# Kernel optimization log

Measured on AMD Instinct MI355X. Metric: run time of the kernel, lower is better.

## Reference

```python
import jax, jax.numpy as jnp
import numpy as np
from jax import lax

B, CIN, COUT, H, W, K = 32, 256, 256, 56, 56, 3

def setup_inputs() -> dict:
    key = jax.random.key(0)
    k1, k2, k3 = jax.random.split(key, 3)
    inp = jax.random.normal(k1, (B, CIN, H, W), dtype=jnp.float32)
    # kaiming-style init for conv kernel, normal init for bias
    fan_in = CIN * K * K
    kernel = jax.random.normal(k2, (COUT, CIN, K, K), dtype=jnp.float32) * np.float32(np.sqrt(2.0 / fan_in))
    bias = jax.random.normal(k3, (COUT,), dtype=jnp.float32)
    return {"inp": inp, "kernel": kernel, "bias": bias}

def reference(inp, kernel, bias):
    # Equivalent to the crossbar path: im2col 3x3 patches @ stacked [kernel|bias]
    # matrix == standard conv2d(padding=1, stride=1) + bias.
    out = lax.conv_general_dilated(
        inp, kernel,
        window_strides=(1, 1),
        padding=((1, 1), (1, 1)),
        dimension_numbers=("NCHW", "OIHW", "NCHW"),
    )
    return out + bias[None, :, None, None]
```

## Files before the change

### kernel.cpp

```cpp
#include <hip/hip_runtime.h>
#include <hip/hip_bf16.h>


#define BB   32
#define CINC 256
#define COUTC 256
#define HH   56
#define WW   56
#define HP   58
#define WP   58
#define PIX_PER_IMG (HH*WW)
#define NPIX (BB*PIX_PER_IMG)
#define KTOT (9*CINC)
#define KB_STEPS (KTOT/32)

#define XT_ELEMS ((size_t)BB*HP*WP*CINC)
#define XT_BYTES (XT_ELEMS*2)
#define WR_ELEMS ((size_t)COUTC*KTOT)
#define WR_BYTES (WR_ELEMS*2)

#define BM 128
#define BN 128
#define BK 32

using frag_t = __attribute__((ext_vector_type(8))) short;
using f32x4  = __attribute__((ext_vector_type(4))) float;

__device__ __forceinline__ void gload_lds16(const void* gsrc, void* ldst) {
  __builtin_amdgcn_global_load_lds(
      (const __attribute__((address_space(1))) unsigned*)gsrc,
      (__attribute__((address_space(3))) unsigned*)ldst, 16, 0, 0);
}

__global__ void xpose_kernel(const float* __restrict__ inp,
                             __hip_bfloat16* __restrict__ xt) {
  int bid = blockIdx.x;
  int hp = bid % HP;
  int t  = bid / HP;
  int cb = t % 4;
  int b  = t / 4;
  __shared__ __hip_bfloat16 tile[64 * 60];
  int tid = threadIdx.x;
  for (int i = tid; i < 64 * 60; i += 256) tile[i] = __float2bfloat16(0.f);
  __syncthreads();
  int h = hp - 1;
  if (h >= 0 && h < HH) {
    const float* src = inp + ((size_t)(b * CINC + cb * 64) * HH + h) * WW;
    for (int i = tid; i < 64 * WW; i += 256) {
      int ci = i / WW, w = i - ci * WW;
      tile[ci * 60 + (w + 1)] = __float2bfloat16(src[(size_t)ci * HH * WW + w]);
    }
  }
  __syncthreads();
  __hip_bfloat16* dst = xt + ((size_t)(b * HP + hp) * WP) * CINC + cb * 64;
  for (int i = tid; i < WP * 64; i += 256) {
    int wp = i >> 6, ci = i & 63;
    dst[(size_t)wp * CINC + ci] = tile[ci * 60 + wp];
  }
}

__global__ void wprep_kernel(const float* __restrict__ k4,
                             __hip_bfloat16* __restrict__ wr) {
  int i = blockIdx.x * 256 + threadIdx.x;
  if (i >= (int)WR_ELEMS) return;
  int co = i / KTOT;
  int k  = i - co * KTOT;
  int tap = k >> 8;
  int ci  = k & 255;
  wr[i] = __float2bfloat16(k4[(co * CINC + ci) * 9 + tap]);
}

__global__ void conv_mfma(const __hip_bfloat16* __restrict__ xt,
                          const __hip_bfloat16* __restrict__ wr,
                          const float* __restrict__ bias,
                          float* __restrict__ out) {
  __shared__ alignas(16) __hip_bfloat16 Alds[BM * BK];
  __shared__ alignas(16) __hip_bfloat16 Blds[BN * BK];

  const int tid  = threadIdx.x;
  const int lane = tid & 63;
  const int wid  = tid >> 6;
  const int wrm  = wid >> 1;
  const int wcn  = wid & 1;
  const int ntile = blockIdx.x;
  const int co0   = blockIdx.y * BM;

  const int qa0 = wid * 128 + lane;
  const int qa1 = qa0 + 64;
  const char* wr_b = (const char*)wr;
  const char* xt_b = (const char*)xt;

  const size_t a_src0 = ((size_t)(co0 + (qa0 >> 2)) * KTOT + (qa0 & 3) * 8) * 2;
  const size_t a_src1 = ((size_t)(co0 + (qa1 >> 2)) * KTOT + (qa1 & 3) * 8) * 2;

  int pxg0 = ntile * BN + (qa0 >> 2);
  int pxg1 = ntile * BN + (qa1 >> 2);
  int b0 = pxg0 / PIX_PER_IMG, hw0 = pxg0 - b0 * PIX_PER_IMG;
  int b1 = pxg1 / PIX_PER_IMG, hw1 = pxg1 - b1 * PIX_PER_IMG;
  int h0 = hw0 / WW, w0 = hw0 - h0 * WW;
  int h1 = hw1 / WW, w1 = hw1 - h1 * WW;
  const size_t b_src0 = ((((size_t)b0 * HP + h0) * WP + w0) * CINC + (qa0 & 3) * 8) * 2;
  const size_t b_src1 = ((((size_t)b1 * HP + h1) * WP + w1) * CINC + (qa1 & 3) * 8) * 2;

  char* a_dst0 = (char*)Alds + (wid * 2) * 1024;
  char* a_dst1 = (char*)Alds + (wid * 2 + 1) * 1024;
  char* b_dst0 = (char*)Blds + (wid * 2) * 1024;
  char* b_dst1 = (char*)Blds + (wid * 2 + 1) * 1024;

  f32x4 acc[4][4] = {};

  const int g  = lane >> 4;
  const int fr = lane & 15;

  for (int kb = 0; kb < KB_STEPS; ++kb) {
    int tap = kb >> 3;
    int r = tap / 3;
    int s = tap - r * 3;
    int ci0 = (kb & 7) * 32;
    size_t aoff = (size_t)kb * 64;
    size_t boff = ((size_t)(r * WP + s) * CINC + ci0) * 2;

    __syncthreads();
    gload_lds16(wr_b + a_src0 + aoff, a_dst0);
    gload_lds16(wr_b + a_src1 + aoff, a_dst1);
    gload_lds16(xt_b + b_src0 + boff, b_dst0);
    gload_lds16(xt_b + b_src1 + boff, b_dst1);
    __syncthreads();

    frag_t a[4], bf[4];
#pragma unroll
    for (int m = 0; m < 4; ++m) {
      int row = wrm * 64 + m * 16 + fr;
      a[m] = *(const frag_t*)((const char*)Alds + row * 64 + g * 16);
    }
#pragma unroll
    for (int n = 0; n < 4; ++n) {
      int row = wcn * 64 + n * 16 + fr;
      bf[n] = *(const frag_t*)((const char*)Blds + row * 64 + g * 16);
    }
#pragma unroll
    for (int m = 0; m < 4; ++m)
#pragma unroll
      for (int n = 0; n < 4; ++n)
        acc[m][n] = __builtin_amdgcn_mfma_f32_16x16x32_bf16(a[m], bf[n], acc[m][n], 0, 0, 0);
  }

  const int fq = lane >> 4;
  int pb[4], phw[4];
#pragma unroll
  for (int n = 0; n < 4; ++n) {
    int pxg = ntile * BN + wcn * 64 + n * 16 + fr;
    pb[n]  = pxg / PIX_PER_IMG;
    phw[n] = pxg - pb[n] * PIX_PER_IMG;
  }
#pragma unroll
  for (int m = 0; m < 4; ++m) {
#pragma unroll
    for (int rg = 0; rg < 4; ++rg) {
      int co = co0 + wrm * 64 + m * 16 + fq * 4 + rg;
      float bv = bias[co];
#pragma unroll
      for (int n = 0; n < 4; ++n) {
        out[((size_t)pb[n] * COUTC + co) * PIX_PER_IMG + phw[n]] = acc[m][n][rg] + bv;
      }
    }
  }
}

__global__ void conv_direct(const float* __restrict__ inp,
                            const float* __restrict__ kern,
                            const float* __restrict__ bias,
                            float* __restrict__ out) {
  int idx = blockIdx.x * 256 + threadIdx.x;
  if (idx >= BB * COUTC * PIX_PER_IMG) return;
  int w = idx % WW;
  int t = idx / WW;
  int h = t % HH; t /= HH;
  int co = t % COUTC;
  int b  = t / COUTC;
  float acc = bias[co];
  for (int ci = 0; ci < CINC; ++ci)
    for (int r = 0; r < 3; ++r) {
      int hh = h + r - 1;
      if (hh < 0 || hh >= HH) continue;
      for (int s = 0; s < 3; ++s) {
        int ww2 = w + s - 1;
        if (ww2 < 0 || ww2 >= WW) continue;
        acc += inp[((size_t)(b * CINC + ci) * HH + hh) * WW + ww2] *
               kern[(co * CINC + ci) * 9 + r * 3 + s];
      }
    }
  out[idx] = acc;
}

extern "C" void kernel_launch(void* const* d_in, const int* in_sizes, int n_in,
                              void* d_out, int out_size, void* d_ws, size_t ws_size,
                              hipStream_t stream) {
  const float* inp  = (const float*)d_in[0];
  const float* kern = (const float*)d_in[1];
  const float* bias = (const float*)d_in[2];
  float* out = (float*)d_out;

  size_t need = XT_BYTES + WR_BYTES;
  if (ws_size < need) {
    int tot = BB * COUTC * PIX_PER_IMG;
    conv_direct<<<(tot + 255) / 256, 256, 0, stream>>>(inp, kern, bias, out);
    return;
  }

  __hip_bfloat16* xt  = (__hip_bfloat16*)d_ws;
  __hip_bfloat16* wrp = (__hip_bfloat16*)((char*)d_ws + XT_BYTES);

  xpose_kernel<<<BB * 4 * HP, 256, 0, stream>>>(inp, xt);
  wprep_kernel<<<(int)((WR_ELEMS + 255) / 256), 256, 0, stream>>>(kern, wrp);
  conv_mfma<<<dim3(NPIX / BN, COUTC / BM), 256, 0, stream>>>(xt, wrp, bias, out);
}
```

Baseline: 209.2 us.

## Rewrite conv GEMM as 256x256 tile, 8-wave, double-buffered swizzled LDS pipeline

Replaces the 128x128 tile, single-buffer implicit-GEMM conv with a 256(Cout)x256(pixel) tile per 512-thread block. It uses BK=64, double-buffered 128KB LDS with an XOR swizzle, and global loads interleaved with MFMA quarters under fine-grained barriers and s_setprio. The aim is to hide global-load latency, cut barrier stalls and LDS bank conflicts, and raise arithmetic intensity per byte loaded. Block IDs are remapped across 8 groups, likely for XCD locality. The cost is heavy LDS use (occupancy of one block per CU) and more register pressure from the 8x4 accumulators.

```diff
diff --git a/kernel.cpp b/kernel.cpp
--- a/kernel.cpp
+++ b/kernel.cpp
@@ -2,26 +2,25 @@
 #include <hip/hip_bf16.h>
 
 
-#define BB   32
-#define CINC 256
+#define BB    32
+#define CINC  256
 #define COUTC 256
-#define HH   56
-#define WW   56
-#define HP   58
-#define WP   58
+#define HH    56
+#define WW    56
+#define HP    58
+#define WP    58
 #define PIX_PER_IMG (HH*WW)
-#define NPIX (BB*PIX_PER_IMG)
-#define KTOT (9*CINC)
-#define KB_STEPS (KTOT/32)
+#define NPIX  (BB*PIX_PER_IMG)
+#define KTOT  (9*CINC)
+#define NKT   36
 
 #define XT_ELEMS ((size_t)BB*HP*WP*CINC)
 #define XT_BYTES (XT_ELEMS*2)
 #define WR_ELEMS ((size_t)COUTC*KTOT)
 #define WR_BYTES (WR_ELEMS*2)
 
-#define BM 128
-#define BN 128
-#define BK 32
+#define LDS_BUF  65536
+#define LDS_BOFF 32768
 
 using frag_t = __attribute__((ext_vector_type(8))) short;
 using f32x4  = __attribute__((ext_vector_type(4))) float;
@@ -70,98 +69,175 @@
   wr[i] = __float2bfloat16(k4[(co * CINC + ci) * 9 + tap]);
 }
 
-__global__ void conv_mfma(const __hip_bfloat16* __restrict__ xt,
-                          const __hip_bfloat16* __restrict__ wr,
-                          const float* __restrict__ bias,
-                          float* __restrict__ out) {
-  __shared__ alignas(16) __hip_bfloat16 Alds[BM * BK];
-  __shared__ alignas(16) __hip_bfloat16 Blds[BN * BK];
+__global__ __launch_bounds__(512, 2) void conv_mfma8(
+    const __hip_bfloat16* __restrict__ xt,
+    const __hip_bfloat16* __restrict__ wr,
+    const float* __restrict__ bias,
+    float* __restrict__ out) {
+  __shared__ alignas(16) char lds[2 * LDS_BUF];
 
   const int tid  = threadIdx.x;
   const int lane = tid & 63;
   const int wid  = tid >> 6;
-  const int wrm  = wid >> 1;
-  const int wcn  = wid & 1;
-  const int ntile = blockIdx.x;
-  const int co0   = blockIdx.y * BM;
-
-  const int qa0 = wid * 128 + lane;
-  const int qa1 = qa0 + 64;
+  const int wm   = wid >> 2;
+  const int wn   = wid & 3;
+  const int fr   = lane & 15;
+  const int g    = lane >> 4;
+
+  const int bid   = blockIdx.x;
+  const int ntile = (bid & 7) * 49 + (bid >> 3);
+
   const char* wr_b = (const char*)wr;
   const char* xt_b = (const char*)xt;
 
-  const size_t a_src0 = ((size_t)(co0 + (qa0 >> 2)) * KTOT + (qa0 & 3) * 8) * 2;
-  const size_t a_src1 = ((size_t)(co0 + (qa1 >> 2)) * KTOT + (qa1 & 3) * 8) * 2;
-
-  int pxg0 = ntile * BN + (qa0 >> 2);
-  int pxg1 = ntile * BN + (qa1 >> 2);
-  int b0 = pxg0 / PIX_PER_IMG, hw0 = pxg0 - b0 * PIX_PER_IMG;
-  int b1 = pxg1 / PIX_PER_IMG, hw1 = pxg1 - b1 * PIX_PER_IMG;
-  int h0 = hw0 / WW, w0 = hw0 - h0 * WW;
-  int h1 = hw1 / WW, w1 = hw1 - h1 * WW;
-  const size_t b_src0 = ((((size_t)b0 * HP + h0) * WP + w0) * CINC + (qa0 & 3) * 8) * 2;
-  const size_t b_src1 = ((((size_t)b1 * HP + h1) * WP + w1) * CINC + (qa1 & 3) * 8) * 2;
-
-  char* a_dst0 = (char*)Alds + (wid * 2) * 1024;
-  char* a_dst1 = (char*)Alds + (wid * 2 + 1) * 1024;
-  char* b_dst0 = (char*)Blds + (wid * 2) * 1024;
-  char* b_dst1 = (char*)Blds + (wid * 2 + 1) * 1024;
-
-  f32x4 acc[4][4] = {};
-
-  const int g  = lane >> 4;
-  const int fr = lane & 15;
-
-  for (int kb = 0; kb < KB_STEPS; ++kb) {
-    int tap = kb >> 3;
-    int r = tap / 3;
-    int s = tap - r * 3;
-    int ci0 = (kb & 7) * 32;
-    size_t aoff = (size_t)kb * 64;
-    size_t boff = ((size_t)(r * WP + s) * CINC + ci0) * 2;
-
-    __syncthreads();
-    gload_lds16(wr_b + a_src0 + aoff, a_dst0);
-    gload_lds16(wr_b + a_src1 + aoff, a_dst1);
-    gload_lds16(xt_b + b_src0 + boff, b_dst0);
-    gload_lds16(xt_b + b_src1 + boff, b_dst1);
-    __syncthreads();
-
-    frag_t a[4], bf[4];
-#pragma unroll
-    for (int m = 0; m < 4; ++m) {
-      int row = wrm * 64 + m * 16 + fr;
-      a[m] = *(const frag_t*)((const char*)Alds + row * 64 + g * 16);
-    }
-#pragma unroll
-    for (int n = 0; n < 4; ++n) {
-      int row = wcn * 64 + n * 16 + fr;
-      bf[n] = *(const frag_t*)((const char*)Blds + row * 64 + g * 16);
-    }
-#pragma unroll
-    for (int m = 0; m < 4; ++m)
-#pragma unroll
-      for (int n = 0; n < 4; ++n)
-        acc[m][n] = __builtin_amdgcn_mfma_f32_16x16x32_bf16(a[m], bf[n], acc[m][n], 0, 0, 0);
-  }
-
-  const int fq = lane >> 4;
+  const int swz   = (((lane & 7) ^ ((lane >> 3) & 7)) << 4);
+  const int lrow8 = lane >> 3;
+
+  const int j0 = wid * 2, j1 = wid * 2 + 1;
+  const int aE0 = ((j0 >> 3) << 4) + (j0 & 7);
+  const int aE1 = ((j1 >> 3) << 4) + (j1 & 7);
+  const int aO0 = aE0 + 8, aO1 = aE1 + 8;
+  const int bE0 = ((j0 >> 2) << 3) + (j0 & 3);
+  const int bE1 = ((j1 >> 2) << 3) + (j1 & 3);
+  const int bO0 = bE0 + 4, bO1 = bE1 + 4;
+
+  const char* pAe0 = wr_b + (size_t)(aE0 * 8 + lrow8) * (KTOT * 2) + swz;
+  const char* pAe1 = wr_b + (size_t)(aE1 * 8 + lrow8) * (KTOT * 2) + swz;
+  const char* pAo0 = wr_b + (size_t)(aO0 * 8 + lrow8) * (KTOT * 2) + swz;
+  const char* pAo1 = wr_b + (size_t)(aO1 * 8 + lrow8) * (KTOT * 2) + swz;
+
+  auto bsrc = [&](int blk) -> const char* {
+    int row = blk * 8 + lrow8;
+    int pxg = ntile * 256 + row;
+    int b  = pxg / PIX_PER_IMG;
+    int hw = pxg - b * PIX_PER_IMG;
+    int h = hw / WW, w = hw - h * WW;
+    return xt_b + (size_t)((b * HP + h) * WP + w) * (CINC * 2) + swz;
+  };
+  const char* pBe0 = bsrc(bE0);
+  const char* pBe1 = bsrc(bE1);
+  const char* pBo0 = bsrc(bO0);
+  const char* pBo1 = bsrc(bO1);
+
+  f32x4 acc[8][4] = {};
+  frag_t afr[4][2], bfr[2][2];
+
+  auto ldA = [&](int bufr, int mh, int m, int kk) -> frag_t {
+    int row = wm * 128 + (mh * 4 + m) * 16 + fr;
+    int c = ((kk << 2) | g) ^ (row & 7);
+    return *(const frag_t*)(lds + bufr + row * 128 + c * 16);
+  };
+  auto ldB = [&](int bufr, int nh, int n, int kk) -> frag_t {
+    int row = wn * 64 + (nh * 2 + n) * 16 + fr;
+    int c = ((kk << 2) | g) ^ (row & 7);
+    return *(const frag_t*)(lds + bufr + LDS_BOFF + row * 128 + c * 16);
+  };
+
+  {
+    char* d = lds;
+    gload_lds16(pAe0, d + aE0 * 1024);
+    gload_lds16(pAe1, d + aE1 * 1024);
+    gload_lds16(pAo0, d + aO0 * 1024);
+    gload_lds16(pAo1, d + aO1 * 1024);
+    gload_lds16(pBe0, d + LDS_BOFF + bE0 * 1024);
+    gload_lds16(pBe1, d + LDS_BOFF + bE1 * 1024);
+    gload_lds16(pBo0, d + LDS_BOFF + bO0 * 1024);
+    gload_lds16(pBo1, d + LDS_BOFF + bO1 * 1024);
+    asm volatile("s_waitcnt vmcnt(0)" ::: "memory");
+    __builtin_amdgcn_s_barrier();
+  }
+
+#define MIDBAR()                                              \
+  asm volatile("s_waitcnt vmcnt(4)" ::: "memory");            \
+  __builtin_amdgcn_s_barrier();                               \
+  asm volatile("s_waitcnt lgkmcnt(0)" ::: "memory");          \
+  __builtin_amdgcn_sched_barrier(0);                          \
+  __builtin_amdgcn_s_setprio(1);
+
+#define ENDBAR()                                              \
+  __builtin_amdgcn_s_setprio(0);                              \
+  __builtin_amdgcn_s_barrier();
+
+#define MFMAQ(MH, NH)                                                          \
+  _Pragma("unroll") for (int kk = 0; kk < 2; ++kk)                             \
+  _Pragma("unroll") for (int m = 0; m < 4; ++m)                                \
+  _Pragma("unroll") for (int n = 0; n < 2; ++n)                                \
+    acc[(MH)*4 + m][(NH)*2 + n] = __builtin_amdgcn_mfma_f32_16x16x32_bf16(     \
+        afr[m][kk], bfr[n][kk], acc[(MH)*4 + m][(NH)*2 + n], 0, 0, 0);
+
+  for (int t = 0; t < NKT; ++t) {
+    const int t1 = (t + 1 < NKT) ? (t + 1) : (NKT - 1);
+    const int bufr = (t & 1) * LDS_BUF;
+    char* ldsw = lds + ((t + 1) & 1) * LDS_BUF;
+    const size_t aoff = (size_t)t1 * 128;
+    const int tap = t1 >> 2;
+    const int rr = tap / 3, ss = tap - rr * 3;
+    const size_t boff = ((size_t)(rr * WP + ss) * CINC + (size_t)(t1 & 3) * 64) * 2;
+
+#pragma unroll
+    for (int kk = 0; kk < 2; ++kk) {
+#pragma unroll
+      for (int m = 0; m < 4; ++m) afr[m][kk] = ldA(bufr, 0, m, kk);
+#pragma unroll
+      for (int n = 0; n < 2; ++n) bfr[n][kk] = ldB(bufr, 0, n, kk);
+    }
+    gload_lds16(pAe0 + aoff, ldsw + aE0 * 1024);
+    gload_lds16(pAe1 + aoff, ldsw + aE1 * 1024);
+    MIDBAR();
+    MFMAQ(0, 0);
+    ENDBAR();
+
+#pragma unroll
+    for (int kk = 0; kk < 2; ++kk)
+#pragma unroll
+      for (int n = 0; n < 2; ++n) bfr[n][kk] = ldB(bufr, 1, n, kk);
+    gload_lds16(pBe0 + boff, ldsw + LDS_BOFF + bE0 * 1024);
+    gload_lds16(pBe1 + boff, ldsw + LDS_BOFF + bE1 * 1024);
+    MIDBAR();
+    MFMAQ(0, 1);
+    ENDBAR();
+
+#pragma unroll
+    for (int kk = 0; kk < 2; ++kk) {
+#pragma unroll
+      for (int m = 0; m < 4; ++m) afr[m][kk] = ldA(bufr, 1, m, kk);
+#pragma unroll
+      for (int n = 0; n < 2; ++n) bfr[n][kk] = ldB(bufr, 0, n, kk);
+    }
+    gload_lds16(pBo0 + boff, ldsw + LDS_BOFF + bO0 * 1024);
+    gload_lds16(pBo1 + boff, ldsw + LDS_BOFF + bO1 * 1024);
+    MIDBAR();
+    MFMAQ(1, 0);
+    ENDBAR();
+
+#pragma unroll
+    for (int kk = 0; kk < 2; ++kk)
+#pragma unroll
+      for (int n = 0; n < 2; ++n) bfr[n][kk] = ldB(bufr, 1, n, kk);
+    gload_lds16(pAo0 + aoff, ldsw + aO0 * 1024);
+    gload_lds16(pAo1 + aoff, ldsw + aO1 * 1024);
+    MIDBAR();
+    MFMAQ(1, 1);
+    ENDBAR();
+  }
+
   int pb[4], phw[4];
 #pragma unroll
-  for (int n = 0; n < 4; ++n) {
-    int pxg = ntile * BN + wcn * 64 + n * 16 + fr;
-    pb[n]  = pxg / PIX_PER_IMG;
-    phw[n] = pxg - pb[n] * PIX_PER_IMG;
-  }
-#pragma unroll
-  for (int m = 0; m < 4; ++m) {
+  for (int nr = 0; nr < 4; ++nr) {
+    int pxg = ntile * 256 + wn * 64 + nr * 16 + fr;
+    pb[nr]  = pxg / PIX_PER_IMG;
+    phw[nr] = pxg - pb[nr] * PIX_PER_IMG;
+  }
+#pragma unroll
+  for (int mr = 0; mr < 8; ++mr) {
 #pragma unroll
     for (int rg = 0; rg < 4; ++rg) {
-      int co = co0 + wrm * 64 + m * 16 + fq * 4 + rg;
+      int co = wm * 128 + mr * 16 + g * 4 + rg;
       float bv = bias[co];
 #pragma unroll
-      for (int n = 0; n < 4; ++n) {
-        out[((size_t)pb[n] * COUTC + co) * PIX_PER_IMG + phw[n]] = acc[m][n][rg] + bv;
+      for (int nr = 0; nr < 4; ++nr) {
+        out[((size_t)pb[nr] * COUTC + co) * PIX_PER_IMG + phw[nr]] =
+            acc[mr][nr][rg] + bv;
       }
     }
   }
@@ -213,5 +289,5 @@
 
   xpose_kernel<<<BB * 4 * HP, 256, 0, stream>>>(inp, xt);
   wprep_kernel<<<(int)((WR_ELEMS + 255) / 256), 256, 0, stream>>>(kern, wrp);
-  conv_mfma<<<dim3(NPIX / BN, COUTC / BM), 256, 0, stream>>>(xt, wrp, bias, out);
-}
+  conv_mfma8<<<NPIX / 256, 512, 0, stream>>>(xt, wrp, bias, out);
+}
```

New measurement: 183.0 us. 1.14x faster.
